# Optimization experiments

Hardware: AMD Instinct MI355X
Metric: run time of the kernel (lower is better)

## Reference

```python
import jax, jax.numpy as jnp
import numpy as np

B, D, O, K = 8192, 256, 256, 16


def setup_inputs() -> dict:
    key = jax.random.key(0)
    k1, k2, k3, k4 = jax.random.split(key, 4)
    x = jax.random.normal(k1, (B, D), dtype=jnp.float32)
    # learned params
    values = jax.random.uniform(k2, (O, D, K), dtype=jnp.float32, minval=-0.05, maxval=0.05)
    skip_w = jax.random.normal(k3, (O, D), dtype=jnp.float32) * (1.0 / np.sqrt(D))
    skip_b = jax.random.uniform(k4, (O,), dtype=jnp.float32, minval=-1.0, maxval=1.0) / np.sqrt(D)
    # fixed buffer (non-trainable)
    grid = jnp.linspace(-1.0, 1.0, K).astype(jnp.float32)
    return {"x": x, "values": values, "skip_w": skip_w, "skip_b": skip_b, "grid": grid}


def reference(x, values, skip_w, skip_b, grid):
    # x: [B, D]; values: [O, D, K]; grid: [K]
    num_knots = grid.shape[0]
    xc = jnp.clip(x, -1.0, 1.0)
    # torch.bucketize(x, grid) (right=False) == searchsorted side='left'
    right = jnp.searchsorted(grid, xc, side="left")            # [B, D]
    left = jnp.clip(right - 1, 0, num_knots - 2)               # [B, D]
    right = left + 1
    g0 = grid[left]
    g1 = grid[right]
    w = (xc - g0) / (g1 - g0 + 1e-12)                          # [B, D]
    # sparse linear-interp coefficients over knots: 2 nonzeros per (b, d)
    coeff = (1.0 - w)[..., None] * jax.nn.one_hot(left, num_knots, dtype=xc.dtype) \
          + w[..., None] * jax.nn.one_hot(right, num_knots, dtype=xc.dtype)  # [B, D, K]
    # y[b,o] = sum_d sum_k coeff[b,d,k] * values[o,d,k]  (== per-dim gather+interp+accumulate)
    y = jnp.einsum("bdk,odk->bo", coeff, values)
    y = y + xc @ skip_w.T + skip_b
    return y
```

## Files before the change

### kernel.cpp

```cpp
#include <hip/hip_runtime.h>
#include <hip/hip_bf16.h>
#include <stdint.h>


#define D_DIM  256
#define O_DIM  256
#define BM     128
#define BK     64
#define NTHR   256

typedef __attribute__((ext_vector_type(8))) short bf16x8;
typedef __attribute__((ext_vector_type(4))) float f32x4;

__global__ __launch_bounds__(256) void kan_prep(
    const float* __restrict__ values,
    const float* __restrict__ skip_w,
    const float* __restrict__ gknots,
    unsigned short* __restrict__ Vp)
{
    int tid = blockIdx.x * blockDim.x + threadIdx.x;
    int e = tid * 8;
    int o = e >> 12;
    int kflat = e & 4095;
    float sw = skip_w[(o << 8) | (kflat >> 4)];
    int kmod = kflat & 15;

    const float4* vp4 = reinterpret_cast<const float4*>(values + e);
    float4 v0 = vp4[0], v1 = vp4[1];
    float f[8] = {v0.x, v0.y, v0.z, v0.w, v1.x, v1.y, v1.z, v1.w};
    unsigned int w[4];
#pragma unroll
    for (int j = 0; j < 4; ++j) {
        float2 ab;
        ab.x = f[2*j]     + gknots[kmod + 2*j]     * sw;
        ab.y = f[2*j + 1] + gknots[kmod + 2*j + 1] * sw;
        __hip_bfloat162 p2 = __float22bfloat162_rn(ab);
        __builtin_memcpy(&w[j], &p2, 4);
    }
    size_t c = (size_t)(kflat >> 3) * 256 + (size_t)o;
    *reinterpret_cast<uint4*>(Vp + c * 8) = make_uint4(w[0], w[1], w[2], w[3]);
}

template<int KS>
__global__ __launch_bounds__(NTHR, 2) void kan_gemm(
    const float* __restrict__ x,
    const unsigned short* __restrict__ Vp,
    float* __restrict__ part)
{
    __shared__ unsigned short As[2][BM * BK];

    constexpr int ITERS = 64 / KS;
    const int t    = threadIdx.x;
    const int lane = t & 63;
    const int wid  = t >> 6;
    const int wm   = wid >> 1;
    const int wn   = wid & 1;
    const int l15  = lane & 15;
    const int lhi  = lane >> 4;

    const int bid = (int)blockIdx.x;
    const int ks  = bid & (KS - 1);
    const int nt  = (bid / KS) & 1;
    const int mt  = bid / (2 * KS);
    const int bm0 = mt * BM;
    const int nc0 = nt * 128;
    const size_t kc0 = (size_t)ks * (512 / KS);

    const int ar  = t >> 1;
    const int ad2 = (t & 1) * 2;
    const float* xp = x + (size_t)(bm0 + ar) * D_DIM + ks * (256 / KS) + ad2;

    char* arow[2] = { (char*)&As[0][0] + ar * 128, (char*)&As[1][0] + ar * 128 };
    const int cs0 = ((2 * ad2)     ^ (ar & 7)) * 16;
    const int cs1 = ((2 * ad2 + 1) ^ (ar & 7)) * 16;
    const int cs2 = ((2 * ad2 + 2) ^ (ar & 7)) * 16;
    const int cs3 = ((2 * ad2 + 3) ^ (ar & 7)) * 16;

    auto buildwd = [&](float xv, unsigned int* wd) {
        float xc = fminf(1.f, fmaxf(-1.f, xv));
        float tt = (xc + 1.f) * 7.5f;
        int li = (int)tt;
        li = li > 14 ? 14 : li;
        float w1 = tt - (float)li;
        float2 cw; cw.x = 1.f - w1; cw.y = w1;
        __hip_bfloat162 p2 = __float22bfloat162_rn(cw);
        unsigned int pk;
        __builtin_memcpy(&pk, &p2, 4);
        unsigned long long w64 = (unsigned long long)pk << ((li & 1) * 16);
        unsigned int lo = (unsigned int)w64;
        unsigned int hi = (unsigned int)(w64 >> 32);
        int jl = li >> 1;
#pragma unroll
        for (int j = 0; j < 8; ++j)
            wd[j] = (j == jl) ? lo : ((j == jl + 1) ? hi : 0u);
    };

    auto stageA = [&](int buf, float2 xv) {
        unsigned int wd[8];
        char* a = arow[buf];
        buildwd(xv.x, wd);
        *reinterpret_cast<uint4*>(a + cs0) = make_uint4(wd[0], wd[1], wd[2], wd[3]);
        *reinterpret_cast<uint4*>(a + cs1) = make_uint4(wd[4], wd[5], wd[6], wd[7]);
        buildwd(xv.y, wd);
        *reinterpret_cast<uint4*>(a + cs2) = make_uint4(wd[0], wd[1], wd[2], wd[3]);
        *reinterpret_cast<uint4*>(a + cs3) = make_uint4(wd[4], wd[5], wd[6], wd[7]);
    };

    #define LOADB(BG, KT)                                                      \
        {                                                                      \
            const unsigned short* _b = Vp + (kc0 + (size_t)(KT) * 8) * 2048;   \
            _Pragma("unroll")                                                  \
            for (int kh = 0; kh < 2; ++kh)                                     \
                _Pragma("unroll")                                              \
                for (int ni = 0; ni < 4; ++ni) {                               \
                    int n = nc0 + wn * 64 + ni * 16 + l15;                     \
                    BG[kh * 4 + ni] = *reinterpret_cast<const bf16x8*>(        \
                        _b + ((size_t)((kh * 4 + lhi) * 256 + n)) * 8);        \
                }                                                              \
        }

    f32x4 acc[4][4] = {};
    bf16x8 bgA[8], bgB[8];

    int abyte[4], a7[4];
#pragma unroll
    for (int mi = 0; mi < 4; ++mi) {
        int m = wm * 64 + mi * 16 + l15;
        abyte[mi] = m * 128;
        a7[mi] = m & 7;
    }

    float2 x1 = *reinterpret_cast<const float2*>(xp);
    LOADB(bgA, 0);
    float2 xn = (ITERS > 1) ? *reinterpret_cast<const float2*>(xp + 4) : x1;
    stageA(0, x1);
    asm volatile("s_waitcnt lgkmcnt(0)" ::: "memory");
    __builtin_amdgcn_s_barrier();
    __builtin_amdgcn_sched_barrier(0);

    #define ITERBODY(KT, CUR, BGC, BGN)                                       \
        {                                                                     \
            const bool last = (KT) == ITERS - 1;                              \
            if (!last) LOADB(BGN, (KT) + 1);                                  \
            const char* Ab = (const char*)&As[CUR][0];                        \
            bf16x8 af[4];                                                     \
                                                                  \
            _Pragma("unroll")                                                 \
            for (int mi = 0; mi < 4; ++mi)                                    \
                af[mi] = *reinterpret_cast<const bf16x8*>(                    \
                    Ab + abyte[mi] + ((lhi ^ a7[mi]) << 4));                  \
            __builtin_amdgcn_s_setprio(1);                                    \
            _Pragma("unroll")                                                 \
            for (int mi = 0; mi < 4; ++mi)                                    \
                _Pragma("unroll")                                             \
                for (int ni = 0; ni < 4; ++ni)                                \
                    acc[mi][ni] = __builtin_amdgcn_mfma_f32_16x16x32_bf16(    \
                        af[mi], BGC[ni], acc[mi][ni], 0, 0, 0);               \
            __builtin_amdgcn_s_setprio(0);                                    \
            if (!last) {                                                      \
                stageA((CUR) ^ 1, xn);                                        \
                if ((KT) + 2 < ITERS)                                         \
                    xn = *reinterpret_cast<const float2*>(xp + ((KT) + 2) * 4);\
            }                                                                 \
                                                                  \
            _Pragma("unroll")                                                 \
            for (int mi = 0; mi < 4; ++mi)                                    \
                af[mi] = *reinterpret_cast<const bf16x8*>(                    \
                    Ab + abyte[mi] + (((4 + lhi) ^ a7[mi]) << 4));            \
            __builtin_amdgcn_s_setprio(1);                                    \
            _Pragma("unroll")                                                 \
            for (int mi = 0; mi < 4; ++mi)                                    \
                _Pragma("unroll")                                             \
                for (int ni = 0; ni < 4; ++ni)                                \
                    acc[mi][ni] = __builtin_amdgcn_mfma_f32_16x16x32_bf16(    \
                        af[mi], BGC[4 + ni], acc[mi][ni], 0, 0, 0);           \
            __builtin_amdgcn_s_setprio(0);                                    \
            if (!last) {                                                      \
                asm volatile("s_waitcnt lgkmcnt(0)" ::: "memory");            \
                __builtin_amdgcn_s_barrier();                                 \
                __builtin_amdgcn_sched_barrier(0);                            \
            }                                                                 \
        }

    for (int t2 = 0; t2 < ITERS / 2; ++t2) {
        ITERBODY(2 * t2,     0, bgA, bgB);
        ITERBODY(2 * t2 + 1, 1, bgB, bgA);
    }
    #undef ITERBODY
    #undef LOADB

    float* dst = part + (size_t)ks * (8192 * 256);
#pragma unroll
    for (int ni = 0; ni < 4; ++ni) {
        int col = nc0 + wn * 64 + ni * 16 + l15;
#pragma unroll
        for (int mi = 0; mi < 4; ++mi) {
            f32x4 v = acc[mi][ni];
            int row0 = bm0 + wm * 64 + mi * 16 + lhi * 4;
#pragma unroll
            for (int r = 0; r < 4; ++r)
                dst[(size_t)(row0 + r) * O_DIM + col] = v[r];
        }
    }
}

__global__ __launch_bounds__(256) void kan_reduce(
    const float* __restrict__ part,
    const float* __restrict__ skip_b,
    float* __restrict__ out,
    int nparts)
{
    size_t i4 = (size_t)blockIdx.x * 256 + threadIdx.x;
    size_t e = i4 * 4;
    f32x4 s = *reinterpret_cast<const f32x4*>(&skip_b[e & 255]);
    for (int p = 0; p < nparts; ++p)
        s += *reinterpret_cast<const f32x4*>(part + (size_t)p * (8192 * 256) + e);
    *reinterpret_cast<f32x4*>(out + e) = s;
}

extern "C" void kernel_launch(void* const* d_in, const int* in_sizes, int n_in,
                              void* d_out, int out_size, void* d_ws, size_t ws_size,
                              hipStream_t stream) {
    const float* x      = (const float*)d_in[0];
    const float* values = (const float*)d_in[1];
    const float* skip_w = (const float*)d_in[2];
    const float* skip_b = (const float*)d_in[3];
    const float* gknots = (const float*)d_in[4];
    float* out = (float*)d_out;
    (void)in_sizes; (void)n_in; (void)out_size;

    unsigned short* Vp = (unsigned short*)d_ws;
    float* part = (float*)((char*)d_ws + 2 * 1024 * 1024);

    kan_prep<<<dim3(512), dim3(256), 0, stream>>>(values, skip_w, gknots, Vp);

    const size_t need4 = 2u * 1024 * 1024 + (size_t)4 * 8192 * 256 * 4;
    if (ws_size >= need4) {
        kan_gemm<4><<<dim3(512), dim3(NTHR), 0, stream>>>(x, Vp, part);
        kan_reduce<<<dim3(2048), dim3(256), 0, stream>>>(part, skip_b, out, 4);
    } else {
        kan_gemm<1><<<dim3(128), dim3(NTHR), 0, stream>>>(x, Vp, out);
        kan_reduce<<<dim3(2048), dim3(256), 0, stream>>>(out, skip_b, out, 1);
    }
}
```

Before: 41.50 us.

## Stage compact knot-index/weight pairs in LDS once and expand A fragments in registers

```diff
diff --git a/kernel.cpp b/kernel.cpp
--- a/kernel.cpp
+++ b/kernel.cpp
@@ -6,7 +6,6 @@
 #define D_DIM  256
 #define O_DIM  256
 #define BM     128
-#define BK     64
 #define NTHR   256
 
 typedef __attribute__((ext_vector_type(8))) short bf16x8;
@@ -47,7 +46,7 @@
     const unsigned short* __restrict__ Vp,
     float* __restrict__ part)
 {
-    __shared__ unsigned short As[2][BM * BK];
+    __shared__ unsigned long long Pk[128 * 64];
 
     constexpr int ITERS = 64 / KS;
     const int t    = threadIdx.x;
@@ -60,51 +59,56 @@
 
     const int bid = (int)blockIdx.x;
     const int ks  = bid & (KS - 1);
-    const int nt  = (bid / KS) & 1;
-    const int mt  = bid / (2 * KS);
+    const int nt  = (bid >> 2) & 1;
+    const int mt  = bid >> 3;
     const int bm0 = mt * BM;
     const int nc0 = nt * 128;
     const size_t kc0 = (size_t)ks * (512 / KS);
 
-    const int ar  = t >> 1;
-    const int ad2 = (t & 1) * 2;
-    const float* xp = x + (size_t)(bm0 + ar) * D_DIM + ks * (256 / KS) + ad2;
-
-    char* arow[2] = { (char*)&As[0][0] + ar * 128, (char*)&As[1][0] + ar * 128 };
-    const int cs0 = ((2 * ad2)     ^ (ar & 7)) * 16;
-    const int cs1 = ((2 * ad2 + 1) ^ (ar & 7)) * 16;
-    const int cs2 = ((2 * ad2 + 2) ^ (ar & 7)) * 16;
-    const int cs3 = ((2 * ad2 + 3) ^ (ar & 7)) * 16;
-
-    auto buildwd = [&](float xv, unsigned int* wd) {
-        float xc = fminf(1.f, fmaxf(-1.f, xv));
-        float tt = (xc + 1.f) * 7.5f;
-        int li = (int)tt;
-        li = li > 14 ? 14 : li;
-        float w1 = tt - (float)li;
-        float2 cw; cw.x = 1.f - w1; cw.y = w1;
-        __hip_bfloat162 p2 = __float22bfloat162_rn(cw);
-        unsigned int pk;
-        __builtin_memcpy(&pk, &p2, 4);
-        unsigned long long w64 = (unsigned long long)pk << ((li & 1) * 16);
-        unsigned int lo = (unsigned int)w64;
-        unsigned int hi = (unsigned int)(w64 >> 32);
-        int jl = li >> 1;
-#pragma unroll
-        for (int j = 0; j < 8; ++j)
-            wd[j] = (j == jl) ? lo : ((j == jl + 1) ? hi : 0u);
-    };
-
-    auto stageA = [&](int buf, float2 xv) {
-        unsigned int wd[8];
-        char* a = arow[buf];
-        buildwd(xv.x, wd);
-        *reinterpret_cast<uint4*>(a + cs0) = make_uint4(wd[0], wd[1], wd[2], wd[3]);
-        *reinterpret_cast<uint4*>(a + cs1) = make_uint4(wd[4], wd[5], wd[6], wd[7]);
-        buildwd(xv.y, wd);
-        *reinterpret_cast<uint4*>(a + cs2) = make_uint4(wd[0], wd[1], wd[2], wd[3]);
-        *reinterpret_cast<uint4*>(a + cs3) = make_uint4(wd[4], wd[5], wd[6], wd[7]);
-    };
+    char* pb = (char*)&Pk[0];
+
+    {
+        int row = t >> 1;
+        int half = (t & 1) * 32;
+        const float* xr = x + (size_t)(bm0 + row) * D_DIM + ks * (256 / KS) + half;
+        int rs = (row & 7) << 2;
+#pragma unroll
+        for (int j4 = 0; j4 < 8; ++j4) {
+            float4 xv = reinterpret_cast<const float4*>(xr)[j4];
+            float v[4] = {xv.x, xv.y, xv.z, xv.w};
+#pragma unroll
+            for (int e = 0; e < 4; ++e) {
+                int dloc = half + j4 * 4 + e;
+                float xc = fminf(1.f, fmaxf(-1.f, v[e]));
+                float tt = (xc + 1.f) * 7.5f;
+                int li = (int)tt;
+                li = li > 14 ? 14 : li;
+                float w1 = tt - (float)li;
+                float2 cw; cw.x = 1.f - w1; cw.y = w1;
+                __hip_bfloat162 p2 = __float22bfloat162_rn(cw);
+                unsigned int pkw;
+                __builtin_memcpy(&pkw, &p2, 4);
+                unsigned long long q8 =
+                    ((unsigned long long)pkw << ((li & 1) << 4)) |
+                    ((unsigned long long)(unsigned)(li >> 1) << 48);
+                int kt = dloc >> 2, p = (dloc >> 1) & 1, g = dloc & 1;
+                int s = kt * 2 + g;
+                *reinterpret_cast<unsigned long long*>(
+                    pb + row * 512 + ((s ^ rs) << 4) + p * 8) = q8;
+            }
+        }
+    }
+    __syncthreads();
+
+    const unsigned jbase = (unsigned)((lhi & 1) * 4);
+    const int g = lhi >> 1;
+    int prow[4], prs[4];
+#pragma unroll
+    for (int mi = 0; mi < 4; ++mi) {
+        int row = wm * 64 + mi * 16 + l15;
+        prow[mi] = row * 512;
+        prs[mi] = (row & 7) << 2;
+    }
 
     #define LOADB(BG, KT)                                                      \
         {                                                                      \
@@ -119,36 +123,37 @@
                 }                                                              \
         }
 
+    auto mkfrag = [&](unsigned lo, unsigned hi) -> bf16x8 {
+        unsigned jd = (hi >> 16) - jbase;
+        unsigned hc = hi & 0xffffu;
+        uint4 w;
+        w.x = (jd == 0u) ? lo : ((jd + 1u == 0u) ? hc : 0u);
+        w.y = (jd == 1u) ? lo : ((jd == 0u) ? hc : 0u);
+        w.z = (jd == 2u) ? lo : ((jd == 1u) ? hc : 0u);
+        w.w = (jd == 3u) ? lo : ((jd == 2u) ? hc : 0u);
+        bf16x8 r;
+        __builtin_memcpy(&r, &w, 16);
+        return r;
+    };
+
     f32x4 acc[4][4] = {};
     bf16x8 bgA[8], bgB[8];
 
-    int abyte[4], a7[4];
-#pragma unroll
-    for (int mi = 0; mi < 4; ++mi) {
-        int m = wm * 64 + mi * 16 + l15;
-        abyte[mi] = m * 128;
-        a7[mi] = m & 7;
-    }
-
-    float2 x1 = *reinterpret_cast<const float2*>(xp);
     LOADB(bgA, 0);
-    float2 xn = (ITERS > 1) ? *reinterpret_cast<const float2*>(xp + 4) : x1;
-    stageA(0, x1);
-    asm volatile("s_waitcnt lgkmcnt(0)" ::: "memory");
-    __builtin_amdgcn_s_barrier();
-    __builtin_amdgcn_sched_barrier(0);
-
-    #define ITERBODY(KT, CUR, BGC, BGN)                                       \
+
+    #define ITERBODY(KT, BGC, BGN)                                            \
         {                                                                     \
             const bool last = (KT) == ITERS - 1;                              \
             if (!last) LOADB(BGN, (KT) + 1);                                  \
-            const char* Ab = (const char*)&As[CUR][0];                        \
+            uint4 q[4];                                                       \
+            _Pragma("unroll")                                                 \
+            for (int mi = 0; mi < 4; ++mi)                                    \
+                q[mi] = *reinterpret_cast<const uint4*>(                      \
+                    pb + prow[mi] + ((((KT) * 2 + g) ^ prs[mi]) << 4));       \
             bf16x8 af[4];                                                     \
-                                                                  \
-            _Pragma("unroll")                                                 \
-            for (int mi = 0; mi < 4; ++mi)                                    \
-                af[mi] = *reinterpret_cast<const bf16x8*>(                    \
-                    Ab + abyte[mi] + ((lhi ^ a7[mi]) << 4));                  \
+            _Pragma("unroll")                                                 \
+            for (int mi = 0; mi < 4; ++mi)                                    \
+                af[mi] = mkfrag(q[mi].x, q[mi].y);                            \
             __builtin_amdgcn_s_setprio(1);                                    \
             _Pragma("unroll")                                                 \
             for (int mi = 0; mi < 4; ++mi)                                    \
@@ -157,16 +162,9 @@
                     acc[mi][ni] = __builtin_amdgcn_mfma_f32_16x16x32_bf16(    \
                         af[mi], BGC[ni], acc[mi][ni], 0, 0, 0);               \
             __builtin_amdgcn_s_setprio(0);                                    \
-            if (!last) {                                                      \
-                stageA((CUR) ^ 1, xn);                                        \
-                if ((KT) + 2 < ITERS)                                         \
-                    xn = *reinterpret_cast<const float2*>(xp + ((KT) + 2) * 4);\
-            }                                                                 \
-                                                                  \
-            _Pragma("unroll")                                                 \
-            for (int mi = 0; mi < 4; ++mi)                                    \
-                af[mi] = *reinterpret_cast<const bf16x8*>(                    \
-                    Ab + abyte[mi] + (((4 + lhi) ^ a7[mi]) << 4));            \
+            _Pragma("unroll")                                                 \
+            for (int mi = 0; mi < 4; ++mi)                                    \
+                af[mi] = mkfrag(q[mi].z, q[mi].w);                            \
             __builtin_amdgcn_s_setprio(1);                                    \
             _Pragma("unroll")                                                 \
             for (int mi = 0; mi < 4; ++mi)                                    \
@@ -175,16 +173,11 @@
                     acc[mi][ni] = __builtin_amdgcn_mfma_f32_16x16x32_bf16(    \
                         af[mi], BGC[4 + ni], acc[mi][ni], 0, 0, 0);           \
             __builtin_amdgcn_s_setprio(0);                                    \
-            if (!last) {                                                      \
-                asm volatile("s_waitcnt lgkmcnt(0)" ::: "memory");            \
-                __builtin_amdgcn_s_barrier();                                 \
-                __builtin_amdgcn_sched_barrier(0);                            \
-            }                                                                 \
         }
 
     for (int t2 = 0; t2 < ITERS / 2; ++t2) {
-        ITERBODY(2 * t2,     0, bgA, bgB);
-        ITERBODY(2 * t2 + 1, 1, bgB, bgA);
+        ITERBODY(2 * t2,     bgA, bgB);
+        ITERBODY(2 * t2 + 1, bgB, bgA);
     }
     #undef ITERBODY
     #undef LOADB
@@ -216,6 +209,30 @@
     for (int p = 0; p < nparts; ++p)
         s += *reinterpret_cast<const f32x4*>(part + (size_t)p * (8192 * 256) + e);
     *reinterpret_cast<f32x4*>(out + e) = s;
+}
+
+__global__ __launch_bounds__(256) void kan_naive(
+    const float* __restrict__ x,
+    const unsigned short* __restrict__ Vp,
+    const float* __restrict__ skip_b,
+    float* __restrict__ out)
+{
+    int b = blockIdx.x, o = threadIdx.x;
+    float acc = skip_b[o];
+    for (int d = 0; d < 256; ++d) {
+        float xc = fminf(1.f, fmaxf(-1.f, x[(size_t)b * 256 + d]));
+        float tt = (xc + 1.f) * 7.5f;
+        int li = (int)tt; li = li > 14 ? 14 : li;
+        float w1 = tt - (float)li;
+        int k0 = d * 16 + li;
+        unsigned short u0 = Vp[((size_t)(k0 >> 3) * 256 + o) * 8 + (k0 & 7)];
+        int k1 = k0 + 1;
+        unsigned short u1 = Vp[((size_t)(k1 >> 3) * 256 + o) * 8 + (k1 & 7)];
+        float f0 = __uint_as_float((unsigned)u0 << 16);
+        float f1 = __uint_as_float((unsigned)u1 << 16);
+        acc += (1.f - w1) * f0 + w1 * f1;
+    }
+    out[(size_t)b * 256 + o] = acc;
 }
 
 extern "C" void kernel_launch(void* const* d_in, const int* in_sizes, int n_in,
@@ -234,12 +251,11 @@
 
     kan_prep<<<dim3(512), dim3(256), 0, stream>>>(values, skip_w, gknots, Vp);
 
-    const size_t need4 = 2u * 1024 * 1024 + (size_t)4 * 8192 * 256 * 4;
-    if (ws_size >= need4) {
+    const size_t need = 2u * 1024 * 1024 + (size_t)4 * 8192 * 256 * 4;
+    if (ws_size >= need) {
         kan_gemm<4><<<dim3(512), dim3(NTHR), 0, stream>>>(x, Vp, part);
         kan_reduce<<<dim3(2048), dim3(256), 0, stream>>>(part, skip_b, out, 4);
     } else {
-        kan_gemm<1><<<dim3(128), dim3(NTHR), 0, stream>>>(x, Vp, out);
-        kan_reduce<<<dim3(2048), dim3(256), 0, stream>>>(out, skip_b, out, 1);
-    }
-}
+        kan_naive<<<dim3(8192), dim3(256), 0, stream>>>(x, Vp, skip_b, out);
+    }
+}
```

Result: slower. 42.40 us (+2.2%).
